# Optimization experiments

Measured on AMD Instinct MI355X. Metric: run time of the kernel, lower is better.

The kernel has to match this reference:

```python
import jax, jax.numpy as jnp
import numpy as np
import math
from jax import lax

N, C, T, V = 32, 128, 400, 27
S, IC = 2, 32
RC = C // 4
EPS = 1e-5


def setup_inputs() -> dict:
    key = jax.random.key(0)
    ks = jax.random.split(key, 24)
    def rn(k, shp, s=0.02):
        return jax.random.normal(k, shp, jnp.float32) * s
    def bnp(k, c):
        g = 1.0 + 0.05 * jax.random.normal(k, (c,), jnp.float32)
        b = 0.05 * jax.random.normal(jax.random.fold_in(k, 1), (c,), jnp.float32)
        return jnp.stack([g, b])  # [2, c] : gamma, beta
    inp = {}
    inp['x'] = jax.random.normal(ks[0], (N, C, T, V), jnp.float32)
    inp['in_w'] = rn(ks[1], (2 * S * IC, C)); inp['in_b'] = rn(ks[2], (2 * S * IC,))
    inp['alphas'] = jnp.ones((1, S, 1, 1), jnp.float32)
    inp['att0'] = jnp.ones((1, S, V, V), jnp.float32) / V
    inp['out_w'] = rn(ks[3], (C, S * C)); inp['out_b'] = rn(ks[4], (C,)); inp['out_bn'] = bnp(ks[5], C)
    inp['ff_w'] = rn(ks[6], (C, C)); inp['ff_b'] = rn(ks[7], (C,)); inp['ff_bn'] = bnp(ks[8], C)
    inp['down_w'] = rn(ks[9], (RC, C)); inp['down_bn'] = bnp(ks[10], RC)
    inp['dw_w'] = rn(ks[11], (3, RC, 3)); inp['dw_b'] = rn(ks[12], (3, RC))
    inp['bn_a'] = jnp.stack([bnp(ks[13], RC), bnp(ks[14], RC), bnp(ks[15], RC)])
    inp['pw_w'] = rn(ks[16], (3, RC, RC))
    inp['bn_b'] = jnp.stack([bnp(ks[17], RC), bnp(ks[18], RC), bnp(ks[19], RC)])
    inp['back_w'] = rn(ks[20], (C, RC)); inp['back_bn'] = bnp(ks[21], C)
    return inp


def conv1x1(x, w, b=None):
    y = jnp.einsum('oc,nctv->notv', w, x)
    if b is not None:
        y = y + b[None, :, None, None]
    return y


def bn(x, p):
    # inference-mode BatchNorm2d with running_mean=0, running_var=1
    scale = p[0] / jnp.sqrt(1.0 + EPS)
    return x * scale[None, :, None, None] + p[1][None, :, None, None]


def lrelu(x):
    return jax.nn.leaky_relu(x, 0.1)


def pos_enc(c, v):
    # PE depends only on joint index (same for every frame)
    pos = jnp.arange(v, dtype=jnp.float32)
    div = jnp.exp(jnp.arange(0, c, 2, dtype=jnp.float32) * (-math.log(10000.0) / c))
    ang = pos[:, None] * div[None, :]                       # [V, C/2]
    pe = jnp.stack([jnp.sin(ang), jnp.cos(ang)], -1).reshape(v, c)  # interleaved sin/cos
    return pe.T[None, :, None, :]                           # [1, C, 1, V]


def reference(x, in_w, in_b, alphas, att0, out_w, out_b, out_bn,
              ff_w, ff_b, ff_bn, down_w, down_bn, dw_w, dw_b,
              bn_a, pw_w, bn_b, back_w, back_bn):
    n, c, t, v = x.shape
    # --- graph self-attention ---
    y = x + pos_enc(c, v)
    qk = conv1x1(y, in_w, in_b).reshape(n, 2 * S, IC, t, v)
    q, k = qk[:, :S], qk[:, S:]
    att = jnp.tanh(jnp.einsum('nsctu,nsctv->nsuv', q, k) / (IC * t)) * alphas + att0
    # dropout identity (eval mode)
    y = jnp.einsum('nctu,nsuv->nsctv', x, att).reshape(n, S * c, t, v)
    y = bn(conv1x1(y, out_w, out_b), out_bn)
    y = lrelu(x + y)               # downs1 = identity (C_in == C_out)
    z = bn(conv1x1(y, ff_w, ff_b), ff_bn)
    y = lrelu(x + z)               # downs2 = identity
    # --- MultiGranularityTemporalConv (stride=1, downt identity) ---
    res = y
    yd = lrelu(bn(conv1x1(y, down_w), down_bn))
    acc = jnp.zeros_like(yd)
    for i, d in enumerate((1, 2, 3)):
        w = dw_w[i][:, None, :, None]  # [RC, 1, 3, 1] depthwise kernel
        h = lax.conv_general_dilated(yd, w, (1, 1), [(d, d), (0, 0)],
                                     rhs_dilation=(d, 1), feature_group_count=RC,
                                     dimension_numbers=('NCHW', 'OIHW', 'NCHW'))
        h = h + dw_b[i][None, :, None, None]
        h = lrelu(bn(h, bn_a[i]))
        acc = acc + bn(conv1x1(h, pw_w[i]), bn_b[i])
    out = bn(conv1x1(acc, back_w), back_bn)
    return lrelu(out + res)
```

## Files before the change

kernel.cpp:

```cpp
#include <hip/hip_runtime.h>
#include <math.h>

#define NN   32
#define CC   128
#define TT   400
#define VV   27
#define SS   2
#define ICC  32
#define RCC  32
#define TVV  (TT * VV)
#define EPSF 1e-5f

static constexpr size_t CTV = (size_t)CC * TVV;
static constexpr size_t FSZ = (size_t)NN * CTV;
static constexpr size_t F4  = (size_t)NN * RCC * TVV;

static constexpr size_t OFF_PE      = 0;
static constexpr size_t OFF_WT_IN   = 4096;
static constexpr size_t OFF_WS_OUT  = 20480;
static constexpr size_t OFF_B_OUT   = 53248;
static constexpr size_t OFF_ZERO    = 53376;
static constexpr size_t OFF_WT_FF   = 53632;
static constexpr size_t OFF_B_FF    = 70016;
static constexpr size_t OFF_WT_DOWN = 70144;
static constexpr size_t OFF_B_DOWN  = 74240;
static constexpr size_t OFF_DWS     = 74272;
static constexpr size_t OFF_DBS     = 74560;
static constexpr size_t OFF_PWS     = 74656;
static constexpr size_t OFF_BSUM    = 77728;
static constexpr size_t OFF_WT_BACK = 77760;
static constexpr size_t OFF_B_BACK  = 81856;
static constexpr size_t OFF_ATT     = 81984;
static constexpr size_t OFF_ATTP    = 128640;
static constexpr size_t OFF_BUFA    = 501888;
static constexpr size_t OFF_YD      = OFF_BUFA + FSZ;
static constexpr size_t OFF_ACC     = OFF_YD + F4;

__global__ void prep_k(const float* __restrict__ in_w,
                       const float* __restrict__ out_w, const float* __restrict__ out_b,
                       const float* __restrict__ out_bn,
                       const float* __restrict__ ff_w, const float* __restrict__ ff_b,
                       const float* __restrict__ ff_bn,
                       const float* __restrict__ down_w, const float* __restrict__ down_bn,
                       const float* __restrict__ dw_w, const float* __restrict__ dw_b,
                       const float* __restrict__ bn_a,
                       const float* __restrict__ pw_w, const float* __restrict__ bn_b,
                       const float* __restrict__ back_w, const float* __restrict__ back_bn,
                       float* __restrict__ ws)
{
  const int gid = blockIdx.x * blockDim.x + threadIdx.x;
  const int nth = gridDim.x * blockDim.x;
  const float rs = rsqrtf(1.f + EPSF);

  for (int i = gid; i < CC * VV; i += nth) {
    const int c = i / VV, v = i % VV;
    const int h = c >> 1;
    const float div = expf((float)(2 * h) * (-logf(10000.f) / (float)CC));
    const float ang = (float)v * div;
    ws[OFF_PE + i] = (c & 1) ? cosf(ang) : sinf(ang);
  }
  for (int i = gid; i < CC * CC; i += nth) {
    const int c = i >> 7, o = i & 127;
    ws[OFF_WT_IN + i] = in_w[o * CC + c];
  }
  for (int i = gid; i < CC * 2 * CC; i += nth) {
    const int c = i >> 8, m = i & 255, o = m & 127, s = m >> 7;
    ws[OFF_WS_OUT + i] = out_w[o * (2 * CC) + s * CC + c] * (out_bn[o] * rs);
  }
  for (int i = gid; i < CC; i += nth) {
    const float s = out_bn[i] * rs;
    ws[OFF_B_OUT + i] = s * out_b[i] + out_bn[CC + i];
  }
  for (int i = gid; i < 256; i += nth) ws[OFF_ZERO + i] = 0.f;
  for (int i = gid; i < CC * CC; i += nth) {
    const int c = i >> 7, o = i & 127;
    ws[OFF_WT_FF + i] = ff_w[o * CC + c] * (ff_bn[o] * rs);
  }
  for (int i = gid; i < CC; i += nth) {
    const float s = ff_bn[i] * rs;
    ws[OFF_B_FF + i] = s * ff_b[i] + ff_bn[CC + i];
  }
  for (int i = gid; i < CC * RCC; i += nth) {
    const int c = i >> 5, o = i & 31;
    ws[OFF_WT_DOWN + i] = down_w[o * CC + c] * (down_bn[o] * rs);
  }
  for (int i = gid; i < RCC; i += nth) ws[OFF_B_DOWN + i] = down_bn[RCC + i];
  for (int i = gid; i < 3 * RCC * 3; i += nth) {
    const int b = i / 96, r = i % 96, c = r / 3;
    ws[OFF_DWS + i] = dw_w[i] * (bn_a[b * 64 + c] * rs);
  }
  for (int i = gid; i < 3 * RCC; i += nth) {
    const int b = i >> 5, c = i & 31;
    ws[OFF_DBS + i] = (bn_a[b * 64 + c] * rs) * dw_b[i] + bn_a[b * 64 + 32 + c];
  }
  for (int i = gid; i < 3 * RCC * RCC; i += nth) {
    const int b = i >> 10, o = (i & 1023) >> 5;
    ws[OFF_PWS + i] = pw_w[i] * (bn_b[b * 64 + o] * rs);
  }
  for (int i = gid; i < RCC; i += nth)
    ws[OFF_BSUM + i] = bn_b[32 + i] + bn_b[96 + i] + bn_b[160 + i];
  for (int i = gid; i < RCC * CC; i += nth) {
    const int k = i >> 7, o = i & 127;
    ws[OFF_WT_BACK + i] = back_w[o * RCC + k] * (back_bn[o] * rs);
  }
  for (int i = gid; i < CC; i += nth) ws[OFF_B_BACK + i] = back_bn[CC + i];
}

template<int M, int K, int TM, int NTHR, bool PE, bool RES, bool LR, bool SPLIT>
__global__ __launch_bounds__(NTHR, 4) void gemm_k(
    const float* __restrict__ X, const float* __restrict__ wT,
    const float* __restrict__ bias, const float* __restrict__ resid,
    const float* __restrict__ pe, float* __restrict__ Y, float* __restrict__ Y2)
{
  __shared__ float Xs[32][68];
  __shared__ float Ws[32][M + 4];
  const int n  = blockIdx.y;
  const int p0 = blockIdx.x * 64;
  const int tid = threadIdx.x;
  const int pg = tid & 15;
  const int og = tid >> 4;

  float acc[TM][4];
#pragma unroll
  for (int i = 0; i < TM; ++i)
#pragma unroll
    for (int j = 0; j < 4; ++j) acc[i][j] = 0.f;

  const float* Xn = X + (size_t)n * K * TVV;

  for (int k0 = 0; k0 < K; k0 += 32) {
    for (int sl = tid; sl < 512; sl += NTHR) {
      const int r  = sl >> 4;
      const int cc = (sl & 15) * 4;
      const int p  = p0 + cc;
      const float* src = Xn + (size_t)(k0 + r) * TVV;
      float4 val;
      if (p + 3 < TVV) {
        val = *(const float4*)(src + p);
      } else {
        val.x = (p     < TVV) ? src[p]     : 0.f;
        val.y = (p + 1 < TVV) ? src[p + 1] : 0.f;
        val.z = (p + 2 < TVV) ? src[p + 2] : 0.f;
        val.w = (p + 3 < TVV) ? src[p + 3] : 0.f;
      }
      if (PE) {
        const float* per = pe + (size_t)(k0 + r) * VV;
        val.x += per[p % VV];
        val.y += per[(p + 1) % VV];
        val.z += per[(p + 2) % VV];
        val.w += per[(p + 3) % VV];
      }
      *(float4*)&Xs[r][cc] = val;
    }
    for (int idx = tid * 4; idx < 32 * M; idx += NTHR * 4) {
      const int rr = idx / M, cw = idx % M;
      *(float4*)&Ws[rr][cw] = *(const float4*)(wT + (size_t)(k0 + rr) * M + cw);
    }
    __syncthreads();
#pragma unroll 8
    for (int k = 0; k < 32; ++k) {
      const float4 xv = *(const float4*)&Xs[k][pg * 4];
      float wv[TM];
      if constexpr (TM == 8) {
        *(float4*)&wv[0] = *(const float4*)&Ws[k][og * 8];
        *(float4*)&wv[4] = *(const float4*)&Ws[k][og * 8 + 4];
      } else if constexpr (TM == 2) {
        *(float2*)&wv[0] = *(const float2*)&Ws[k][og * 2];
      } else {
#pragma unroll
        for (int i = 0; i < TM; ++i) wv[i] = Ws[k][og * TM + i];
      }
#pragma unroll
      for (int i = 0; i < TM; ++i) {
        acc[i][0] = fmaf(wv[i], xv.x, acc[i][0]);
        acc[i][1] = fmaf(wv[i], xv.y, acc[i][1]);
        acc[i][2] = fmaf(wv[i], xv.z, acc[i][2]);
        acc[i][3] = fmaf(wv[i], xv.w, acc[i][3]);
      }
    }
    __syncthreads();
  }

  const size_t baseR = (size_t)n * CTV;
  const int pcol = p0 + pg * 4;
#pragma unroll
  for (int i = 0; i < TM; ++i) {
    const int o = og * TM + i;
    const float bv = bias[o];
    float* dst;
    size_t rowoff;
    if constexpr (SPLIT) {
      dst = (o < CC) ? Y : Y2;
      rowoff = (size_t)n * CTV + (size_t)(o & (CC - 1)) * TVV;
    } else {
      dst = Y;
      rowoff = (size_t)n * ((size_t)M * TVV) + (size_t)o * TVV;
    }
    if (pcol + 3 < TVV) {
      float4 st;
      st.x = acc[i][0] + bv; st.y = acc[i][1] + bv;
      st.z = acc[i][2] + bv; st.w = acc[i][3] + bv;
      if (RES) {
        const float4 rr4 = *(const float4*)(resid + baseR + (size_t)o * TVV + pcol);
        st.x += rr4.x; st.y += rr4.y; st.z += rr4.z; st.w += rr4.w;
      }
      if (LR) {
        st.x = st.x > 0.f ? st.x : 0.1f * st.x;
        st.y = st.y > 0.f ? st.y : 0.1f * st.y;
        st.z = st.z > 0.f ? st.z : 0.1f * st.z;
        st.w = st.w > 0.f ? st.w : 0.1f * st.w;
      }
      *(float4*)(dst + rowoff + pcol) = st;
    } else {
#pragma unroll
      for (int j = 0; j < 4; ++j) {
        const int p = pcol + j;
        if (p < TVV) {
          float v = acc[i][j] + bv;
          if (RES) v += resid[baseR + (size_t)o * TVV + p];
          if (LR)  v = v > 0.f ? v : 0.1f * v;
          dst[rowoff + p] = v;
        }
      }
    }
  }
}

__global__ __launch_bounds__(256) void attpart_k(
    const float* __restrict__ qk, float* __restrict__ attP)
{
  __shared__ float qs[270], ks[270];
  const int ns  = blockIdx.x;
  const int seg = blockIdx.y;
  const int n = ns >> 1, s = ns & 1;
  const int tid = threadIdx.x;
  const float* qb = qk + (size_t)n * CTV + (size_t)(s * ICC) * TVV;
  const float* kb = qk + (size_t)n * CTV + (size_t)((SS + s) * ICC) * TVV;
  const int p0 = tid, p1 = tid + 256, p2 = tid + 512;
  const int u0 = p0 / VV, v0 = p0 % VV;
  const int u1 = p1 / VV, v1 = p1 % VV;
  const int u2 = p2 / VV, v2 = p2 % VV;
  float a0 = 0.f, a1 = 0.f, a2 = 0.f;
  for (int c = 0; c < ICC; ++c) {
    const float* qrow = qb + (size_t)c * TVV;
    const float* krow = kb + (size_t)c * TVV;
    for (int t0 = seg * 50; t0 < seg * 50 + 50; t0 += 10) {
      for (int idx = tid; idx < 270; idx += 256) {
        qs[idx] = qrow[t0 * VV + idx];
        ks[idx] = krow[t0 * VV + idx];
      }
      __syncthreads();
#pragma unroll
      for (int tt = 0; tt < 10; ++tt) {
        const float* qr = &qs[tt * VV];
        const float* kr = &ks[tt * VV];
        a0 = fmaf(qr[u0], kr[v0], a0);
        a1 = fmaf(qr[u1], kr[v1], a1);
        if (p2 < 729) a2 = fmaf(qr[u2], kr[v2], a2);
      }
      __syncthreads();
    }
  }
  float* dst = attP + (size_t)seg * (NN * SS * VV * VV) + (size_t)ns * (VV * VV);
  dst[p0] = a0;
  dst[p1] = a1;
  if (p2 < 729) dst[p2] = a2;
}

__global__ void attfin_k(const float* __restrict__ attP,
                         const float* __restrict__ alphas,
                         const float* __restrict__ att0,
                         float* __restrict__ att)
{
  const int idx = blockIdx.x * 256 + threadIdx.x;
  if (idx >= NN * SS * VV * VV) return;
  float m = 0.f;
#pragma unroll
  for (int g = 0; g < 8; ++g) m += attP[(size_t)g * (NN * SS * VV * VV) + idx];
  const int s  = (idx / (VV * VV)) & 1;
  const int uv = idx % (VV * VV);
  att[idx] = tanhf(m * (1.f / (ICC * TT))) * alphas[s] + att0[s * VV * VV + uv];
}

__global__ __launch_bounds__(256, 4) void attapply_k(
    const float* __restrict__ x, const float* __restrict__ z0,
    float* __restrict__ z1y, const float* __restrict__ att,
    const float* __restrict__ bO)
{
  __shared__ float zs[256][29];
  __shared__ float as[SS][VV][28];
  const int n    = blockIdx.y;
  const int row0 = blockIdx.x * 256;
  const int tid  = threadIdx.x;

  for (int i = tid; i < SS * VV * VV; i += 256) {
    const int s = i / (VV * VV), uv = i % (VV * VV);
    as[s][uv / VV][uv % VV] = att[(size_t)n * (SS * VV * VV) + i];
  }
  for (int i = tid; i < SS * VV; i += 256) as[i / VV][i % VV][27] = 0.f;

  float acc[28];
#pragma unroll
  for (int j = 0; j < 28; ++j) acc[j] = 0.f;

  const size_t base = (size_t)n * CTV + (size_t)row0 * VV;

  for (int s = 0; s < SS; ++s) {
    const float* zsrc = (s == 0 ? z0 : (const float*)z1y) + base;
    __syncthreads();
    for (int e = tid; e < 256 * VV; e += 256) zs[e / VV][e % VV] = zsrc[e];
    __syncthreads();
    float zr[VV];
#pragma unroll
    for (int u = 0; u < VV; ++u) zr[u] = zs[tid][u];
#pragma unroll
    for (int vg = 0; vg < 7; ++vg) {
#pragma unroll
      for (int u = 0; u < VV; ++u) {
        const float4 a4 = *(const float4*)&as[s][u][vg * 4];
        acc[vg * 4 + 0] = fmaf(zr[u], a4.x, acc[vg * 4 + 0]);
        acc[vg * 4 + 1] = fmaf(zr[u], a4.y, acc[vg * 4 + 1]);
        acc[vg * 4 + 2] = fmaf(zr[u], a4.z, acc[vg * 4 + 2]);
        acc[vg * 4 + 3] = fmaf(zr[u], a4.w, acc[vg * 4 + 3]);
      }
    }
  }

  const int o  = (row0 + tid) / TT;
  const float bv = bO[o];
  __syncthreads();
#pragma unroll
  for (int v = 0; v < VV; ++v) zs[tid][v] = acc[v] + bv;
  __syncthreads();
  for (int e = tid; e < 256 * VV; e += 256) {
    float val = zs[e / VV][e % VV] + x[base + e];
    val = val > 0.f ? val : 0.1f * val;
    z1y[base + e] = val;
  }
}

__global__ __launch_bounds__(256, 2) void tcn_k(
    const float* __restrict__ yd, const float* __restrict__ dws,
    const float* __restrict__ dbs, const float* __restrict__ pws,
    const float* __restrict__ bsum, float* __restrict__ accO)
{
  __shared__ float Ys[RCC][10][VV];
  __shared__ float Hs[RCC * 4 * VV];
  const int n  = blockIdx.y;
  const int t0 = blockIdx.x * 4;
  const int tid = threadIdx.x;
  const float* yb = yd + (size_t)n * RCC * TVV;

  for (int idx = tid; idx < RCC * 10 * VV; idx += 256) {
    const int c  = idx / (10 * VV);
    const int rr = (idx / VV) % 10;
    const int v  = idx % VV;
    const int t  = t0 - 3 + rr;
    Ys[c][rr][v] = (t >= 0 && t < TT) ? yb[(size_t)c * TVV + (size_t)t * VV + v] : 0.f;
  }
  __syncthreads();

  float accr[14];
#pragma unroll
  for (int j = 0; j < 14; ++j) accr[j] = 0.f;

  for (int i = 0; i < 3; ++i) {
    const int d = i + 1;
    for (int idx = tid; idx < RCC * 4 * VV; idx += 256) {
      const int c  = idx / (4 * VV);
      const int rr = idx % (4 * VV);
      const int t2 = rr / VV;
      const int v  = rr % VV;
      const float* w = dws + (size_t)(i * RCC + c) * 3;
      float h = dbs[i * RCC + c]
              + w[0] * Ys[c][3 + t2 - d][v]
              + w[1] * Ys[c][3 + t2][v]
              + w[2] * Ys[c][3 + t2 + d][v];
      Hs[idx] = h > 0.f ? h : 0.1f * h;
    }
    __syncthreads();
#pragma unroll
    for (int j = 0; j < 14; ++j) {
      const int idx = tid + j * 256;
      if (idx < RCC * 4 * VV) {
        const int o  = idx / (4 * VV);
        const int rr = idx % (4 * VV);
        const float* pwrow = pws + (size_t)(i * RCC + o) * RCC;
        const float* hc = &Hs[rr];
        float a = accr[j];
#pragma unroll 8
        for (int c = 0; c < RCC; ++c) a = fmaf(pwrow[c], hc[c * 4 * VV], a);
        accr[j] = a;
      }
    }
    __syncthreads();
  }
#pragma unroll
  for (int j = 0; j < 14; ++j) {
    const int idx = tid + j * 256;
    if (idx < RCC * 4 * VV) {
      const int o  = idx / (4 * VV);
      const int rr = idx % (4 * VV);
      const int t2 = rr / VV;
      const int v  = rr % VV;
      accO[(size_t)n * RCC * TVV + (size_t)o * TVV + (size_t)(t0 + t2) * VV + v]
          = accr[j] + bsum[o];
    }
  }
}

extern "C" void kernel_launch(void* const* d_in, const int* in_sizes, int n_in,
                              void* d_out, int out_size, void* d_ws, size_t ws_size,
                              hipStream_t stream)
{
  const float* x       = (const float*)d_in[0];
  const float* in_w    = (const float*)d_in[1];
  const float* in_b    = (const float*)d_in[2];
  const float* alphas  = (const float*)d_in[3];
  const float* att0    = (const float*)d_in[4];
  const float* out_w   = (const float*)d_in[5];
  const float* out_b   = (const float*)d_in[6];
  const float* out_bn  = (const float*)d_in[7];
  const float* ff_w    = (const float*)d_in[8];
  const float* ff_b    = (const float*)d_in[9];
  const float* ff_bn   = (const float*)d_in[10];
  const float* down_w  = (const float*)d_in[11];
  const float* down_bn = (const float*)d_in[12];
  const float* dw_w    = (const float*)d_in[13];
  const float* dw_b    = (const float*)d_in[14];
  const float* bn_a    = (const float*)d_in[15];
  const float* pw_w    = (const float*)d_in[16];
  const float* bn_b    = (const float*)d_in[17];
  const float* back_w  = (const float*)d_in[18];
  const float* back_bn = (const float*)d_in[19];
  float* ws  = (float*)d_ws;
  float* out = (float*)d_out;

  prep_k<<<64, 256, 0, stream>>>(in_w, out_w, out_b, out_bn, ff_w, ff_b, ff_bn,
                                 down_w, down_bn, dw_w, dw_b, bn_a, pw_w, bn_b,
                                 back_w, back_bn, ws);
  gemm_k<128, 128, 8, 256, true, false, false, false><<<dim3(169, 32), 256, 0, stream>>>(
      x, ws + OFF_WT_IN, in_b, nullptr, ws + OFF_PE, ws + OFF_BUFA, nullptr);
  attpart_k<<<dim3(64, 8), 256, 0, stream>>>(ws + OFF_BUFA, ws + OFF_ATTP);
  attfin_k<<<(NN * SS * VV * VV + 255) / 256, 256, 0, stream>>>(
      ws + OFF_ATTP, alphas, att0, ws + OFF_ATT);
  gemm_k<256, 128, 8, 512, false, false, false, true><<<dim3(169, 32), 512, 0, stream>>>(
      x, ws + OFF_WS_OUT, ws + OFF_ZERO, nullptr, nullptr, ws + OFF_BUFA, out);
  attapply_k<<<dim3(200, 32), 256, 0, stream>>>(
      x, ws + OFF_BUFA, out, ws + OFF_ATT, ws + OFF_B_OUT);
  gemm_k<128, 128, 8, 256, false, true, true, false><<<dim3(169, 32), 256, 0, stream>>>(
      out, ws + OFF_WT_FF, ws + OFF_B_FF, x, nullptr, ws + OFF_BUFA, nullptr);
  gemm_k<32, 128, 2, 256, false, false, true, false><<<dim3(169, 32), 256, 0, stream>>>(
      ws + OFF_BUFA, ws + OFF_WT_DOWN, ws + OFF_B_DOWN, nullptr, nullptr, ws + OFF_YD, nullptr);
  tcn_k<<<dim3(100, 32), 256, 0, stream>>>(
      ws + OFF_YD, ws + OFF_DWS, ws + OFF_DBS, ws + OFF_PWS, ws + OFF_BSUM, ws + OFF_ACC);
  gemm_k<128, 32, 8, 256, false, true, true, false><<<dim3(169, 32), 256, 0, stream>>>(
      ws + OFF_ACC, ws + OFF_WT_BACK, ws + OFF_B_BACK, ws + OFF_BUFA, nullptr, out, nullptr);
}
```

Baseline: 1.774 ms.

## Fuse out-projection with attention mix, ff with down, and TCN with back conv

Replaces the generic templated GEMM pipeline with three fused kernels. The output projection is fused with the attention mix and residual/leaky-ReLU, so the 2x-size intermediate z never goes to global memory. The ff conv is fused with the down projection, and the temporal conv block is fused with the back projection and final residual. This removes several full-tensor HBM round trips and kernel launches, at the cost of higher register and shared-memory pressure and lower occupancy in the fused kernels.

```diff
diff --git a/kernel.cpp b/kernel.cpp
--- a/kernel.cpp
+++ b/kernel.cpp
@@ -19,7 +19,6 @@
 static constexpr size_t OFF_WT_IN   = 4096;
 static constexpr size_t OFF_WS_OUT  = 20480;
 static constexpr size_t OFF_B_OUT   = 53248;
-static constexpr size_t OFF_ZERO    = 53376;
 static constexpr size_t OFF_WT_FF   = 53632;
 static constexpr size_t OFF_B_FF    = 70016;
 static constexpr size_t OFF_WT_DOWN = 70144;
@@ -34,7 +33,6 @@
 static constexpr size_t OFF_ATTP    = 128640;
 static constexpr size_t OFF_BUFA    = 501888;
 static constexpr size_t OFF_YD      = OFF_BUFA + FSZ;
-static constexpr size_t OFF_ACC     = OFF_YD + F4;
 
 __global__ void prep_k(const float* __restrict__ in_w,
                        const float* __restrict__ out_w, const float* __restrict__ out_b,
@@ -71,7 +69,6 @@
     const float s = out_bn[i] * rs;
     ws[OFF_B_OUT + i] = s * out_b[i] + out_bn[CC + i];
   }
-  for (int i = gid; i < 256; i += nth) ws[OFF_ZERO + i] = 0.f;
   for (int i = gid; i < CC * CC; i += nth) {
     const int c = i >> 7, o = i & 127;
     ws[OFF_WT_FF + i] = ff_w[o * CC + c] * (ff_bn[o] * rs);
@@ -106,30 +103,29 @@
   for (int i = gid; i < CC; i += nth) ws[OFF_B_BACK + i] = back_bn[CC + i];
 }
 
-template<int M, int K, int TM, int NTHR, bool PE, bool RES, bool LR, bool SPLIT>
-__global__ __launch_bounds__(NTHR, 4) void gemm_k(
+__global__ __launch_bounds__(256, 4) void qkproj_k(
     const float* __restrict__ X, const float* __restrict__ wT,
-    const float* __restrict__ bias, const float* __restrict__ resid,
-    const float* __restrict__ pe, float* __restrict__ Y, float* __restrict__ Y2)
+    const float* __restrict__ bias, const float* __restrict__ pe,
+    float* __restrict__ Y)
 {
   __shared__ float Xs[32][68];
-  __shared__ float Ws[32][M + 4];
+  __shared__ float Ws[32][132];
   const int n  = blockIdx.y;
   const int p0 = blockIdx.x * 64;
   const int tid = threadIdx.x;
   const int pg = tid & 15;
   const int og = tid >> 4;
 
-  float acc[TM][4];
-#pragma unroll
-  for (int i = 0; i < TM; ++i)
+  float acc[8][4];
+#pragma unroll
+  for (int i = 0; i < 8; ++i)
 #pragma unroll
     for (int j = 0; j < 4; ++j) acc[i][j] = 0.f;
 
-  const float* Xn = X + (size_t)n * K * TVV;
-
-  for (int k0 = 0; k0 < K; k0 += 32) {
-    for (int sl = tid; sl < 512; sl += NTHR) {
+  const float* Xn = X + (size_t)n * CTV;
+
+  for (int k0 = 0; k0 < CC; k0 += 32) {
+    for (int sl = tid; sl < 512; sl += 256) {
       const int r  = sl >> 4;
       const int cc = (sl & 15) * 4;
       const int p  = p0 + cc;
@@ -143,35 +139,26 @@
         val.z = (p + 2 < TVV) ? src[p + 2] : 0.f;
         val.w = (p + 3 < TVV) ? src[p + 3] : 0.f;
       }
-      if (PE) {
-        const float* per = pe + (size_t)(k0 + r) * VV;
-        val.x += per[p % VV];
-        val.y += per[(p + 1) % VV];
-        val.z += per[(p + 2) % VV];
-        val.w += per[(p + 3) % VV];
-      }
+      const float* per = pe + (size_t)(k0 + r) * VV;
+      val.x += per[p % VV];
+      val.y += per[(p + 1) % VV];
+      val.z += per[(p + 2) % VV];
+      val.w += per[(p + 3) % VV];
       *(float4*)&Xs[r][cc] = val;
     }
-    for (int idx = tid * 4; idx < 32 * M; idx += NTHR * 4) {
-      const int rr = idx / M, cw = idx % M;
-      *(float4*)&Ws[rr][cw] = *(const float4*)(wT + (size_t)(k0 + rr) * M + cw);
+    for (int q = tid; q < 1024; q += 256) {
+      const int r = q >> 5, c4 = (q & 31) * 4;
+      *(float4*)&Ws[r][c4] = *(const float4*)(wT + (size_t)(k0 + r) * CC + c4);
     }
     __syncthreads();
 #pragma unroll 8
     for (int k = 0; k < 32; ++k) {
       const float4 xv = *(const float4*)&Xs[k][pg * 4];
-      float wv[TM];
-      if constexpr (TM == 8) {
-        *(float4*)&wv[0] = *(const float4*)&Ws[k][og * 8];
-        *(float4*)&wv[4] = *(const float4*)&Ws[k][og * 8 + 4];
-      } else if constexpr (TM == 2) {
-        *(float2*)&wv[0] = *(const float2*)&Ws[k][og * 2];
-      } else {
-#pragma unroll
-        for (int i = 0; i < TM; ++i) wv[i] = Ws[k][og * TM + i];
-      }
-#pragma unroll
-      for (int i = 0; i < TM; ++i) {
+      const float4 wA = *(const float4*)&Ws[k][og * 8];
+      const float4 wB = *(const float4*)&Ws[k][og * 8 + 4];
+      const float wv[8] = {wA.x, wA.y, wA.z, wA.w, wB.x, wB.y, wB.z, wB.w};
+#pragma unroll
+      for (int i = 0; i < 8; ++i) {
         acc[i][0] = fmaf(wv[i], xv.x, acc[i][0]);
         acc[i][1] = fmaf(wv[i], xv.y, acc[i][1]);
         acc[i][2] = fmaf(wv[i], xv.z, acc[i][2]);
@@ -181,46 +168,22 @@
     __syncthreads();
   }
 
-  const size_t baseR = (size_t)n * CTV;
   const int pcol = p0 + pg * 4;
 #pragma unroll
-  for (int i = 0; i < TM; ++i) {
-    const int o = og * TM + i;
+  for (int i = 0; i < 8; ++i) {
+    const int o = og * 8 + i;
     const float bv = bias[o];
-    float* dst;
-    size_t rowoff;
-    if constexpr (SPLIT) {
-      dst = (o < CC) ? Y : Y2;
-      rowoff = (size_t)n * CTV + (size_t)(o & (CC - 1)) * TVV;
-    } else {
-      dst = Y;
-      rowoff = (size_t)n * ((size_t)M * TVV) + (size_t)o * TVV;
-    }
+    const size_t rowoff = (size_t)n * CTV + (size_t)o * TVV;
     if (pcol + 3 < TVV) {
       float4 st;
       st.x = acc[i][0] + bv; st.y = acc[i][1] + bv;
       st.z = acc[i][2] + bv; st.w = acc[i][3] + bv;
-      if (RES) {
-        const float4 rr4 = *(const float4*)(resid + baseR + (size_t)o * TVV + pcol);
-        st.x += rr4.x; st.y += rr4.y; st.z += rr4.z; st.w += rr4.w;
-      }
-      if (LR) {
-        st.x = st.x > 0.f ? st.x : 0.1f * st.x;
-        st.y = st.y > 0.f ? st.y : 0.1f * st.y;
-        st.z = st.z > 0.f ? st.z : 0.1f * st.z;
-        st.w = st.w > 0.f ? st.w : 0.1f * st.w;
-      }
-      *(float4*)(dst + rowoff + pcol) = st;
+      *(float4*)(Y + rowoff + pcol) = st;
     } else {
 #pragma unroll
       for (int j = 0; j < 4; ++j) {
         const int p = pcol + j;
-        if (p < TVV) {
-          float v = acc[i][j] + bv;
-          if (RES) v += resid[baseR + (size_t)o * TVV + p];
-          if (LR)  v = v > 0.f ? v : 0.1f * v;
-          dst[rowoff + p] = v;
-        }
+        if (p < TVV) Y[rowoff + p] = acc[i][j] + bv;
       }
     }
   }
@@ -282,81 +245,286 @@
   att[idx] = tanhf(m * (1.f / (ICC * TT))) * alphas[s] + att0[s * VV * VV + uv];
 }
 
-__global__ __launch_bounds__(256, 4) void attapply_k(
-    const float* __restrict__ x, const float* __restrict__ z0,
-    float* __restrict__ z1y, const float* __restrict__ att,
-    const float* __restrict__ bO)
-{
-  __shared__ float zs[256][29];
-  __shared__ float as[SS][VV][28];
-  const int n    = blockIdx.y;
-  const int row0 = blockIdx.x * 256;
-  const int tid  = threadIdx.x;
-
-  for (int i = tid; i < SS * VV * VV; i += 256) {
+__global__ __launch_bounds__(576, 4) void zmix_k(
+    const float* __restrict__ x, const float* __restrict__ wT,
+    const float* __restrict__ att, const float* __restrict__ bO,
+    float* __restrict__ y1)
+{
+  __shared__ float SM[14848];
+  __shared__ float as[SS * VV * 28];
+  const int n   = blockIdx.y;
+  const int p0  = blockIdx.x * 108;
+  const int tid = threadIdx.x;
+
+  for (int i = tid; i < SS * VV * VV; i += 576) {
     const int s = i / (VV * VV), uv = i % (VV * VV);
-    as[s][uv / VV][uv % VV] = att[(size_t)n * (SS * VV * VV) + i];
-  }
-  for (int i = tid; i < SS * VV; i += 256) as[i / VV][i % VV][27] = 0.f;
-
-  float acc[28];
-#pragma unroll
-  for (int j = 0; j < 28; ++j) acc[j] = 0.f;
-
-  const size_t base = (size_t)n * CTV + (size_t)row0 * VV;
-
-  for (int s = 0; s < SS; ++s) {
-    const float* zsrc = (s == 0 ? z0 : (const float*)z1y) + base;
-    __syncthreads();
-    for (int e = tid; e < 256 * VV; e += 256) zs[e / VV][e % VV] = zsrc[e];
-    __syncthreads();
-    float zr[VV];
-#pragma unroll
-    for (int u = 0; u < VV; ++u) zr[u] = zs[tid][u];
-#pragma unroll
-    for (int vg = 0; vg < 7; ++vg) {
-#pragma unroll
-      for (int u = 0; u < VV; ++u) {
-        const float4 a4 = *(const float4*)&as[s][u][vg * 4];
-        acc[vg * 4 + 0] = fmaf(zr[u], a4.x, acc[vg * 4 + 0]);
-        acc[vg * 4 + 1] = fmaf(zr[u], a4.y, acc[vg * 4 + 1]);
-        acc[vg * 4 + 2] = fmaf(zr[u], a4.z, acc[vg * 4 + 2]);
-        acc[vg * 4 + 3] = fmaf(zr[u], a4.w, acc[vg * 4 + 3]);
-      }
-    }
-  }
-
-  const int o  = (row0 + tid) / TT;
-  const float bv = bO[o];
+    as[s * VV * 28 + (uv / VV) * 28 + (uv % VV)] = att[(size_t)n * (SS * VV * VV) + i];
+  }
+
+  const int og = tid / 18;
+  const int pg = tid % 18;
+
+  float acc[8][6];
+#pragma unroll
+  for (int i = 0; i < 8; ++i)
+#pragma unroll
+    for (int j = 0; j < 6; ++j) acc[i][j] = 0.f;
+
+  const float* Xn = x + (size_t)n * CTV;
+  float* Xs = SM;
+  float* Ws = SM + 3584;
+
+  for (int k0 = 0; k0 < CC; k0 += 32) {
+    for (int q = tid; q < 864; q += 576) {
+      const int r = q / 27, c4 = (q % 27) * 4;
+      *(float4*)&Xs[r * 112 + c4] =
+          *(const float4*)(Xn + (size_t)(k0 + r) * TVV + p0 + c4);
+    }
+    for (int q = tid; q < 2048; q += 576) {
+      const int r = q >> 6, c4 = (q & 63) * 4;
+      *(float4*)&Ws[r * 260 + c4] = *(const float4*)(wT + (size_t)(k0 + r) * 256 + c4);
+    }
+    __syncthreads();
+#pragma unroll 4
+    for (int k = 0; k < 32; ++k) {
+      const float* xr = &Xs[k * 112 + pg * 6];
+      const float2 x01 = *(const float2*)(xr);
+      const float2 x23 = *(const float2*)(xr + 2);
+      const float2 x45 = *(const float2*)(xr + 4);
+      const float xv[6] = {x01.x, x01.y, x23.x, x23.y, x45.x, x45.y};
+      const float4 wA = *(const float4*)&Ws[k * 260 + og * 8];
+      const float4 wB = *(const float4*)&Ws[k * 260 + og * 8 + 4];
+      const float wv[8] = {wA.x, wA.y, wA.z, wA.w, wB.x, wB.y, wB.z, wB.w};
+#pragma unroll
+      for (int i = 0; i < 8; ++i)
+#pragma unroll
+        for (int j = 0; j < 6; ++j)
+          acc[i][j] = fmaf(wv[i], xv[j], acc[i][j]);
+    }
+    __syncthreads();
+  }
+
+  float* zs = SM;
+  const int tl = pg / 9;
+  const int v0 = pg * 3 - tl * 27;
+  const size_t nbase = (size_t)n * CTV;
+
+  for (int t2 = 0; t2 < 2; ++t2) {
+    __syncthreads();
+    if (pg >= t2 * 9 && pg < t2 * 9 + 9) {
+      const int pl = (pg - t2 * 9) * 6;
+#pragma unroll
+      for (int i = 0; i < 8; ++i) {
+        float* zrow = &zs[(og * 8 + i) * 58 + pl];
+        *(float2*)(zrow)     = make_float2(acc[i][0], acc[i][1]);
+        *(float2*)(zrow + 2) = make_float2(acc[i][2], acc[i][3]);
+        *(float2*)(zrow + 4) = make_float2(acc[i][4], acc[i][5]);
+      }
+    }
+    __syncthreads();
+
+    float y[4][3];
+#pragma unroll
+    for (int oi = 0; oi < 4; ++oi)
+      y[oi][0] = y[oi][1] = y[oi][2] = 0.f;
+
+    const float* a0 = &as[v0];
+    const float* a1 = &as[VV * 28 + v0];
+    const int ur = tl * 27;
+#pragma unroll 9
+    for (int u = 0; u < 27; ++u) {
+      const float a00 = a0[u * 28], a01 = a0[u * 28 + 1], a02 = a0[u * 28 + 2];
+      const float a10 = a1[u * 28], a11 = a1[u * 28 + 1], a12 = a1[u * 28 + 2];
+#pragma unroll
+      for (int oi = 0; oi < 4; ++oi) {
+        const float z0 = zs[(og * 4 + oi) * 58 + ur + u];
+        const float z1 = zs[(128 + og * 4 + oi) * 58 + ur + u];
+        y[oi][0] = fmaf(z0, a00, fmaf(z1, a10, y[oi][0]));
+        y[oi][1] = fmaf(z0, a01, fmaf(z1, a11, y[oi][1]));
+        y[oi][2] = fmaf(z0, a02, fmaf(z1, a12, y[oi][2]));
+      }
+    }
+    const int t = p0 / 27 + t2 * 2 + tl;
+#pragma unroll
+    for (int oi = 0; oi < 4; ++oi) {
+      const int o = og * 4 + oi;
+      const size_t addr = nbase + (size_t)o * TVV + (size_t)t * VV + v0;
+      const float bv = bO[o];
+#pragma unroll
+      for (int j = 0; j < 3; ++j) {
+        float val = y[oi][j] + bv + x[addr + j];
+        val = val > 0.f ? val : 0.1f * val;
+        y1[addr + j] = val;
+      }
+    }
+  }
+}
+
+__global__ __launch_bounds__(256, 3) void ffdown_k(
+    const float* __restrict__ y1, const float* __restrict__ wT,
+    const float* __restrict__ bF, const float* __restrict__ xres,
+    const float* __restrict__ wdT, const float* __restrict__ bD,
+    float* __restrict__ y2, float* __restrict__ yd)
+{
+  __shared__ float SM[13056];
+  const int n  = blockIdx.y;
+  const int p0 = blockIdx.x * 64;
+  const int tid = threadIdx.x;
+  const int pg = tid & 15;
+  const int og = tid >> 4;
+
+  float acc[8][4];
+#pragma unroll
+  for (int i = 0; i < 8; ++i)
+#pragma unroll
+    for (int j = 0; j < 4; ++j) acc[i][j] = 0.f;
+
+  float* Xs = SM;
+  float* Ws = SM + 2176;
+  const float* Xn = y1 + (size_t)n * CTV;
+
+  for (int k0 = 0; k0 < CC; k0 += 32) {
+    for (int sl = tid; sl < 512; sl += 256) {
+      const int r  = sl >> 4;
+      const int cc = (sl & 15) * 4;
+      const int p  = p0 + cc;
+      const float* src = Xn + (size_t)(k0 + r) * TVV;
+      float4 val;
+      if (p + 3 < TVV) {
+        val = *(const float4*)(src + p);
+      } else {
+        val.x = (p     < TVV) ? src[p]     : 0.f;
+        val.y = (p + 1 < TVV) ? src[p + 1] : 0.f;
+        val.z = (p + 2 < TVV) ? src[p + 2] : 0.f;
+        val.w = (p + 3 < TVV) ? src[p + 3] : 0.f;
+      }
+      *(float4*)&Xs[r * 68 + cc] = val;
+    }
+    for (int q = tid; q < 1024; q += 256) {
+      const int r = q >> 5, c4 = (q & 31) * 4;
+      *(float4*)&Ws[r * 132 + c4] = *(const float4*)(wT + (size_t)(k0 + r) * CC + c4);
+    }
+    __syncthreads();
+#pragma unroll 8
+    for (int k = 0; k < 32; ++k) {
+      const float4 xv = *(const float4*)&Xs[k * 68 + pg * 4];
+      const float4 wA = *(const float4*)&Ws[k * 132 + og * 8];
+      const float4 wB = *(const float4*)&Ws[k * 132 + og * 8 + 4];
+      const float wv[8] = {wA.x, wA.y, wA.z, wA.w, wB.x, wB.y, wB.z, wB.w};
+#pragma unroll
+      for (int i = 0; i < 8; ++i) {
+        acc[i][0] = fmaf(wv[i], xv.x, acc[i][0]);
+        acc[i][1] = fmaf(wv[i], xv.y, acc[i][1]);
+        acc[i][2] = fmaf(wv[i], xv.z, acc[i][2]);
+        acc[i][3] = fmaf(wv[i], xv.w, acc[i][3]);
+      }
+    }
+    __syncthreads();
+  }
+
+  float* y2s = SM;
+  float* wds = SM + 8704;
+  const size_t nb = (size_t)n * CTV;
+  const int pcol = p0 + pg * 4;
+
+  for (int q = tid; q < 2048; q += 256) {
+    const int c = q >> 4, o2 = (q & 15) * 2;
+    *(float2*)&wds[c * 34 + o2] = *(const float2*)(wdT + c * 32 + o2);
+  }
+#pragma unroll
+  for (int i = 0; i < 8; ++i) {
+    const int o = og * 8 + i;
+    const float bv = bF[o];
+    const size_t rowoff = nb + (size_t)o * TVV;
+    if (pcol + 3 < TVV) {
+      const float4 rr4 = *(const float4*)(xres + rowoff + pcol);
+      float4 st;
+      st.x = acc[i][0] + bv + rr4.x;
+      st.y = acc[i][1] + bv + rr4.y;
+      st.z = acc[i][2] + bv + rr4.z;
+      st.w = acc[i][3] + bv + rr4.w;
+      st.x = st.x > 0.f ? st.x : 0.1f * st.x;
+      st.y = st.y > 0.f ? st.y : 0.1f * st.y;
+      st.z = st.z > 0.f ? st.z : 0.1f * st.z;
+      st.w = st.w > 0.f ? st.w : 0.1f * st.w;
+      *(float4*)(y2 + rowoff + pcol) = st;
+      *(float4*)&y2s[o * 68 + pg * 4] = st;
+    } else {
+#pragma unroll
+      for (int j = 0; j < 4; ++j) {
+        const int p = pcol + j;
+        float v = 0.f;
+        if (p < TVV) {
+          v = acc[i][j] + bv + xres[rowoff + p];
+          v = v > 0.f ? v : 0.1f * v;
+          y2[rowoff + p] = v;
+        }
+        y2s[o * 68 + pg * 4 + j] = v;
+      }
+    }
+  }
   __syncthreads();
-#pragma unroll
-  for (int v = 0; v < VV; ++v) zs[tid][v] = acc[v] + bv;
-  __syncthreads();
-  for (int e = tid; e < 256 * VV; e += 256) {
-    float val = zs[e / VV][e % VV] + x[base + e];
-    val = val > 0.f ? val : 0.1f * val;
-    z1y[base + e] = val;
-  }
-}
-
-__global__ __launch_bounds__(256, 2) void tcn_k(
+
+  float d0[4] = {0.f, 0.f, 0.f, 0.f};
+  float d1[4] = {0.f, 0.f, 0.f, 0.f};
+  const int o2g = og;
+#pragma unroll 4
+  for (int c = 0; c < CC; ++c) {
+    const float4 yv = *(const float4*)&y2s[c * 68 + pg * 4];
+    const float2 w  = *(const float2*)&wds[c * 34 + o2g * 2];
+    d0[0] = fmaf(w.x, yv.x, d0[0]); d0[1] = fmaf(w.x, yv.y, d0[1]);
+    d0[2] = fmaf(w.x, yv.z, d0[2]); d0[3] = fmaf(w.x, yv.w, d0[3]);
+    d1[0] = fmaf(w.y, yv.x, d1[0]); d1[1] = fmaf(w.y, yv.y, d1[1]);
+    d1[2] = fmaf(w.y, yv.z, d1[2]); d1[3] = fmaf(w.y, yv.w, d1[3]);
+  }
+  const size_t ydb = (size_t)n * RCC * TVV;
+#pragma unroll
+  for (int oi = 0; oi < 2; ++oi) {
+    const int o2 = o2g * 2 + oi;
+    const float bv = bD[o2];
+    float* dv = oi ? d1 : d0;
+    if (pcol + 3 < TVV) {
+      float4 st;
+      st.x = dv[0] + bv; st.y = dv[1] + bv; st.z = dv[2] + bv; st.w = dv[3] + bv;
+      st.x = st.x > 0.f ? st.x : 0.1f * st.x;
+      st.y = st.y > 0.f ? st.y : 0.1f * st.y;
+      st.z = st.z > 0.f ? st.z : 0.1f * st.z;
+      st.w = st.w > 0.f ? st.w : 0.1f * st.w;
+      *(float4*)(yd + ydb + (size_t)o2 * TVV + pcol) = st;
+    } else {
+#pragma unroll
+      for (int j = 0; j < 4; ++j) {
+        const int p = pcol + j;
+        if (p < TVV) {
+          float v = dv[j] + bv;
+          v = v > 0.f ? v : 0.1f * v;
+          yd[ydb + (size_t)o2 * TVV + p] = v;
+        }
+      }
+    }
+  }
+}
+
+__global__ __launch_bounds__(256, 3) void tcnback_k(
     const float* __restrict__ yd, const float* __restrict__ dws,
     const float* __restrict__ dbs, const float* __restrict__ pws,
-    const float* __restrict__ bsum, float* __restrict__ accO)
-{
-  __shared__ float Ys[RCC][10][VV];
-  __shared__ float Hs[RCC * 4 * VV];
+    const float* __restrict__ bsum, const float* __restrict__ wbT,
+    const float* __restrict__ bB, const float* __restrict__ y2,
+    float* __restrict__ out)
+{
+  __shared__ float SM[12224];
   const int n  = blockIdx.y;
   const int t0 = blockIdx.x * 4;
   const int tid = threadIdx.x;
+  float* Ys = SM;
+  float* Hs = SM + 8640;
+
   const float* yb = yd + (size_t)n * RCC * TVV;
-
   for (int idx = tid; idx < RCC * 10 * VV; idx += 256) {
-    const int c  = idx / (10 * VV);
-    const int rr = (idx / VV) % 10;
-    const int v  = idx % VV;
-    const int t  = t0 - 3 + rr;
-    Ys[c][rr][v] = (t >= 0 && t < TT) ? yb[(size_t)c * TVV + (size_t)t * VV + v] : 0.f;
+    const int c = idx / 270, rr = (idx / 27) % 10, v = idx % 27;
+    const int t = t0 - 3 + rr;
+    Ys[c * 270 + rr * 27 + v] =
+        (t >= 0 && t < TT) ? yb[(size_t)c * TVV + (size_t)t * VV + v] : 0.f;
   }
   __syncthreads();
 
@@ -366,45 +534,80 @@
 
   for (int i = 0; i < 3; ++i) {
     const int d = i + 1;
-    for (int idx = tid; idx < RCC * 4 * VV; idx += 256) {
-      const int c  = idx / (4 * VV);
-      const int rr = idx % (4 * VV);
-      const int t2 = rr / VV;
-      const int v  = rr % VV;
+    for (int idx = tid; idx < 3456; idx += 256) {
+      const int c = idx / 108, rr = idx % 108, t2 = rr / 27, v = rr % 27;
       const float* w = dws + (size_t)(i * RCC + c) * 3;
       float h = dbs[i * RCC + c]
-              + w[0] * Ys[c][3 + t2 - d][v]
-              + w[1] * Ys[c][3 + t2][v]
-              + w[2] * Ys[c][3 + t2 + d][v];
+              + w[0] * Ys[c * 270 + (3 + t2 - d) * 27 + v]
+              + w[1] * Ys[c * 270 + (3 + t2) * 27 + v]
+              + w[2] * Ys[c * 270 + (3 + t2 + d) * 27 + v];
       Hs[idx] = h > 0.f ? h : 0.1f * h;
     }
     __syncthreads();
 #pragma unroll
     for (int j = 0; j < 14; ++j) {
       const int idx = tid + j * 256;
-      if (idx < RCC * 4 * VV) {
-        const int o  = idx / (4 * VV);
-        const int rr = idx % (4 * VV);
+      if (idx < 3456) {
+        const int o = idx / 108, rr = idx % 108;
         const float* pwrow = pws + (size_t)(i * RCC + o) * RCC;
-        const float* hc = &Hs[rr];
         float a = accr[j];
 #pragma unroll 8
-        for (int c = 0; c < RCC; ++c) a = fmaf(pwrow[c], hc[c * 4 * VV], a);
+        for (int c = 0; c < RCC; ++c) a = fmaf(pwrow[c], Hs[c * 108 + rr], a);
         accr[j] = a;
       }
     }
     __syncthreads();
   }
+
+  float* accs = SM;
+  float* wbs  = SM + 3584;
 #pragma unroll
   for (int j = 0; j < 14; ++j) {
     const int idx = tid + j * 256;
-    if (idx < RCC * 4 * VV) {
-      const int o  = idx / (4 * VV);
-      const int rr = idx % (4 * VV);
-      const int t2 = rr / VV;
-      const int v  = rr % VV;
-      accO[(size_t)n * RCC * TVV + (size_t)o * TVV + (size_t)(t0 + t2) * VV + v]
-          = accr[j] + bsum[o];
+    if (idx < 3456) {
+      const int o = idx / 108, rr = idx % 108, t2 = rr / 27, v = rr % 27;
+      accs[o * 112 + t2 * 28 + v] = accr[j] + bsum[o];
+    }
+  }
+  for (int q = tid; q < 128; q += 256)
+    accs[(q >> 2) * 112 + (q & 3) * 28 + 27] = 0.f;
+  for (int q = tid; q < 4096; q += 256) wbs[q] = wbT[q];
+  __syncthreads();
+
+  const int og3 = tid >> 2, tg = tid & 3;
+  const int o0 = og3 * 2;
+  float yy[2][28];
+#pragma unroll
+  for (int v = 0; v < 28; ++v) { yy[0][v] = 0.f; yy[1][v] = 0.f; }
+#pragma unroll 4
+  for (int k = 0; k < 32; ++k) {
+    const float2 w = *(const float2*)&wbs[k * 128 + o0];
+    const float* ar = &accs[k * 112 + tg * 28];
+#pragma unroll
+    for (int v4 = 0; v4 < 7; ++v4) {
+      const float4 a = *(const float4*)&ar[v4 * 4];
+      yy[0][v4 * 4 + 0] = fmaf(w.x, a.x, yy[0][v4 * 4 + 0]);
+      yy[0][v4 * 4 + 1] = fmaf(w.x, a.y, yy[0][v4 * 4 + 1]);
+      yy[0][v4 * 4 + 2] = fmaf(w.x, a.z, yy[0][v4 * 4 + 2]);
+      yy[0][v4 * 4 + 3] = fmaf(w.x, a.w, yy[0][v4 * 4 + 3]);
+      yy[1][v4 * 4 + 0] = fmaf(w.y, a.x, yy[1][v4 * 4 + 0]);
+      yy[1][v4 * 4 + 1] = fmaf(w.y, a.y, yy[1][v4 * 4 + 1]);
+      yy[1][v4 * 4 + 2] = fmaf(w.y, a.z, yy[1][v4 * 4 + 2]);
+      yy[1][v4 * 4 + 3] = fmaf(w.y, a.w, yy[1][v4 * 4 + 3]);
+    }
+  }
+  const size_t ob = (size_t)n * CTV;
+  const int t = t0 + tg;
+#pragma unroll
+  for (int oi = 0; oi < 2; ++oi) {
+    const int o = o0 + oi;
+    const float bb = bB[o];
+    const size_t addr = ob + (size_t)o * TVV + (size_t)t * VV;
+#pragma unroll
+    for (int v = 0; v < 27; ++v) {
+      float val = yy[oi][v] + bb + y2[addr + v];
+      val = val > 0.f ? val : 0.1f * val;
+      out[addr + v] = val;
     }
   }
 }
@@ -439,21 +642,17 @@
   prep_k<<<64, 256, 0, stream>>>(in_w, out_w, out_b, out_bn, ff_w, ff_b, ff_bn,
                                  down_w, down_bn, dw_w, dw_b, bn_a, pw_w, bn_b,
                                  back_w, back_bn, ws);
-  gemm_k<128, 128, 8, 256, true, false, false, false><<<dim3(169, 32), 256, 0, stream>>>(
-      x, ws + OFF_WT_IN, in_b, nullptr, ws + OFF_PE, ws + OFF_BUFA, nullptr);
+  qkproj_k<<<dim3(169, 32), 256, 0, stream>>>(
+      x, ws + OFF_WT_IN, in_b, ws + OFF_PE, ws + OFF_BUFA);
   attpart_k<<<dim3(64, 8), 256, 0, stream>>>(ws + OFF_BUFA, ws + OFF_ATTP);
   attfin_k<<<(NN * SS * VV * VV + 255) / 256, 256, 0, stream>>>(
       ws + OFF_ATTP, alphas, att0, ws + OFF_ATT);
-  gemm_k<256, 128, 8, 512, false, false, false, true><<<dim3(169, 32), 512, 0, stream>>>(
-      x, ws + OFF_WS_OUT, ws + OFF_ZERO, nullptr, nullptr, ws + OFF_BUFA, out);
-  attapply_k<<<dim3(200, 32), 256, 0, stream>>>(
-      x, ws + OFF_BUFA, out, ws + OFF_ATT, ws + OFF_B_OUT);
-  gemm_k<128, 128, 8, 256, false, true, true, false><<<dim3(169, 32), 256, 0, stream>>>(
-      out, ws + OFF_WT_FF, ws + OFF_B_FF, x, nullptr, ws + OFF_BUFA, nullptr);
-  gemm_k<32, 128, 2, 256, false, false, true, false><<<dim3(169, 32), 256, 0, stream>>>(
-      ws + OFF_BUFA, ws + OFF_WT_DOWN, ws + OFF_B_DOWN, nullptr, nullptr, ws + OFF_YD, nullptr);
-  tcn_k<<<dim3(100, 32), 256, 0, stream>>>(
-      ws + OFF_YD, ws + OFF_DWS, ws + OFF_DBS, ws + OFF_PWS, ws + OFF_BSUM, ws + OFF_ACC);
-  gemm_k<128, 32, 8, 256, false, true, true, false><<<dim3(169, 32), 256, 0, stream>>>(
-      ws + OFF_ACC, ws + OFF_WT_BACK, ws + OFF_B_BACK, ws + OFF_BUFA, nullptr, out, nullptr);
-}
+  zmix_k<<<dim3(100, 32), 576, 0, stream>>>(
+      x, ws + OFF_WS_OUT, ws + OFF_ATT, ws + OFF_B_OUT, out);
+  ffdown_k<<<dim3(169, 32), 256, 0, stream>>>(
+      out, ws + OFF_WT_FF, ws + OFF_B_FF, x, ws + OFF_WT_DOWN, ws + OFF_B_DOWN,
+      ws + OFF_BUFA, ws + OFF_YD);
+  tcnback_k<<<dim3(100, 32), 256, 0, stream>>>(
+      ws + OFF_YD, ws + OFF_DWS, ws + OFF_DBS, ws + OFF_PWS, ws + OFF_BSUM,
+      ws + OFF_WT_BACK, ws + OFF_B_BACK, ws + OFF_BUFA, out);
+}
```

New measurement: 1.907 ms. +7.5%, slower.
